# Kernel optimization log

Measured on AMD Instinct MI355X. Metric: run time of the kernel, lower is better.

Reference implementation:

```python
import jax, jax.numpy as jnp
import numpy as np

BN_EPS = 1e-5


def three_nn(unknown, known):
    # squared pairwise distances via gemm form: ||u||^2 + ||k||^2 - 2 u.k
    # unknown: (B, n, 3), known: (B, m, 3) -> d: (B, n, m)
    u2 = jnp.sum(unknown * unknown, axis=-1, keepdims=True)          # (B, n, 1)
    k2 = jnp.sum(known * known, axis=-1)[:, None, :]                 # (B, 1, m)
    d = u2 + k2 - 2.0 * jnp.einsum('bnc,bmc->bnm', unknown, known)   # (B, n, m)
    neg_d, idx = jax.lax.top_k(-d, 3)                                # 3 smallest
    return -neg_d, idx                                               # (B,n,3), (B,n,3) int32


def three_interpolate(known_feats, idx, weight):
    # known_feats: (B, C, m), idx/weight: (B, n, 3) -> (B, C, n)
    g = jnp.take_along_axis(known_feats[:, :, None, :], idx[:, None, :, :], axis=3)  # (B,C,n,3)
    return jnp.sum(g * weight[:, None, :, :], axis=3)


def conv1x1(x, W, b):
    # x: (B, C_in, N), W: (C_out, C_in), b: (C_out,)
    return jnp.einsum('oc,bcn->bon', W, x) + b[None, :, None]


def batchnorm(x, gamma, beta):
    # training-mode BN over (B, N) per channel, biased variance
    mean = jnp.mean(x, axis=(0, 2), keepdims=True)
    var = jnp.mean((x - mean) ** 2, axis=(0, 2), keepdims=True)
    xn = (x - mean) * jax.lax.rsqrt(var + BN_EPS)
    return xn * gamma[None, :, None] + beta[None, :, None]


def setup_inputs() -> dict:
    key = jax.random.key(0)
    ks = jax.random.split(key, 16)
    B, n, m = 16, 4096, 1024
    C1, C2, C = 128, 256, 256  # in_channels, known feat channels (=mlp[0]), mlp width
    inp = {
        'unknown': jax.random.normal(ks[0], (B, n, 3), jnp.float32),
        'known': jax.random.normal(ks[1], (B, m, 3), jnp.float32),
        'unknow_feats': jax.random.normal(ks[2], (B, C1, n), jnp.float32),
        'known_feats': jax.random.normal(ks[3], (B, C2, m), jnp.float32),
        # mlp_unknow: Conv1d(C1->C) + BN (no relu)
        'Wu': jax.random.normal(ks[4], (C, C1), jnp.float32) * (1.0 / np.sqrt(C1)),
        'bu': jnp.zeros((C,), jnp.float32),
        'gu': jnp.ones((C,), jnp.float32),
        'betau': jnp.zeros((C,), jnp.float32),
        # mlp_convs[0]: Conv1d(C->C) + BN + relu
        'W1': jax.random.normal(ks[5], (C, C), jnp.float32) * (1.0 / np.sqrt(C)),
        'b1': jnp.zeros((C,), jnp.float32),
        'g1': jnp.ones((C,), jnp.float32),
        'beta1': jnp.zeros((C,), jnp.float32),
        # mlp_convs[1]: Conv1d(C->C) + BN + relu
        'W2': jax.random.normal(ks[6], (C, C), jnp.float32) * (1.0 / np.sqrt(C)),
        'b2': jnp.zeros((C,), jnp.float32),
        'g2': jnp.ones((C,), jnp.float32),
        'beta2': jnp.zeros((C,), jnp.float32),
    }
    return inp


def reference(unknown, known, unknow_feats, known_feats,
              Wu, bu, gu, betau, W1, b1, g1, beta1, W2, b2, g2, beta2):
    dist, idx = three_nn(unknown, known)            # squared dists (B,n,3)
    dist_recip = 1.0 / (dist + 1e-8)
    norm = jnp.sum(dist_recip, axis=2, keepdims=True)
    weight = dist_recip / norm
    interpolated = three_interpolate(known_feats, idx, weight)   # (B, 256, n)

    skip = batchnorm(conv1x1(unknow_feats, Wu, bu), gu, betau)   # (B, 256, n)
    x = interpolated + skip
    x = jax.nn.relu(batchnorm(conv1x1(x, W1, b1), g1, beta1))
    x = jax.nn.relu(batchnorm(conv1x1(x, W2, b2), g2, beta2))
    return x
```

## Files before the change

### kernel.cpp

```cpp
#include <hip/hip_runtime.h>
#include <hip/hip_bf16.h>
#include <cstddef>
#include <cstdint>

#define BATCH 16
#define NPTS  4096
#define MPTS  1024
#define PTOT  65536
#define C1    128
#define C2    256

typedef short bf16x8 __attribute__((ext_vector_type(8)));
typedef float f32x4  __attribute__((ext_vector_type(4)));
typedef unsigned int u32x4 __attribute__((ext_vector_type(4)));

static __device__ __forceinline__ float bf2f(unsigned int u16) {
    union { unsigned int i; float f; } v; v.i = u16 << 16; return v.f;
}
static __device__ __forceinline__ unsigned short f2bf(float f) {
    union { float f; unsigned int i; } v; v.f = f;
    unsigned int u = v.i;
    return (unsigned short)((u + 0x7FFFu + ((u >> 16) & 1u)) >> 16);
}

static __device__ __forceinline__ void st_wt_b128(void* p, u32x4 v) {
    asm volatile("global_store_dwordx4 %0, %1, off sc0 sc1" :: "v"(p), "v"(v) : "memory");
}
static __device__ __forceinline__ void st_wt_f128(void* p, f32x4 v) {
    asm volatile("global_store_dwordx4 %0, %1, off sc0 sc1" :: "v"(p), "v"(v) : "memory");
}
static __device__ __forceinline__ void st_wt_b64(void* p, uint2 v) {
    asm volatile("global_store_dwordx2 %0, %1, off sc0 sc1" :: "v"(p), "v"(v) : "memory");
}
static __device__ __forceinline__ void st_wt_b32(void* p, unsigned v) {
    asm volatile("global_store_dword %0, %1, off sc0 sc1" :: "v"(p), "v"(v) : "memory");
}
static __device__ __forceinline__ void st_wt_b16(void* p, unsigned v) {
    asm volatile("global_store_short %0, %1, off sc0 sc1" :: "v"(p), "v"(v) : "memory");
}

template <int SWZ>
__global__ void k_transpose(const float* __restrict__ in, unsigned short* __restrict__ out,
                            int C, int N) {
    __shared__ float tile[64][65];
    int b  = blockIdx.z;
    int n0 = blockIdx.x * 64;
    int c0 = blockIdx.y * 64;
    const float* src = in + (size_t)b * C * N;
    unsigned short* dst = out + (size_t)b * N * C;
    int t  = threadIdx.x;
    int t4 = t >> 6;
    int tn = t & 63;
#pragma unroll
    for (int i = 0; i < 16; ++i) {
        int cc = i * 4 + t4;
        tile[cc][tn] = src[(size_t)(c0 + cc) * N + n0 + tn];
    }
    __syncthreads();
#pragma unroll
    for (int i = 0; i < 16; ++i) {
        int nn = i * 4 + t4;
        int p  = n0 + nn;
        int c  = c0 + tn;
        size_t off;
        if (SWZ) off = (size_t)p * C + (size_t)((((c >> 3) ^ (p & 7)) << 3) + (c & 7));
        else     off = (size_t)p * C + c;
        st_wt_b16(dst + off, (unsigned)f2bf(tile[tn][nn]));
    }
}

__global__ void k_cvt_pack(const float* __restrict__ in, unsigned short* __restrict__ out, int K) {
    int tid = blockIdx.x * 256 + threadIdx.x;
    if (tid >= 256 * K) return;
    int ch = tid / K, k = tid % K;
    int ks = k >> 5, lhi = (k >> 3) & 3, e = k & 7;
    int wv = ch >> 6, i = (ch >> 4) & 3, llo = ch & 15;
    int lane = lhi * 16 + llo;
    st_wt_b16(out + ((size_t)((ks * 16 + wv * 4 + i) * 64 + lane)) * 8 + e,
              (unsigned)f2bf(in[tid]));
}

static __device__ __forceinline__ bool nn_less(float da, int ia, float db, int ib) {
    return (da < db) || (da == db && ia < ib);
}

__global__ void k_three_nn(const float* __restrict__ unknown, const float* __restrict__ known,
                           int* __restrict__ idx_out, float* __restrict__ w_out) {
    __shared__ float4 kpt[MPTS + 4];
    int t  = threadIdx.x;
    int p0 = blockIdx.x * 64;
    int b  = p0 >> 12;
    const float* kb = known + (size_t)b * MPTS * 3;
    for (int i = t; i < MPTS; i += 256) {
        float x = kb[i * 3 + 0], y = kb[i * 3 + 1], z = kb[i * 3 + 2];
        float dd = __fadd_rn(__fadd_rn(__fmul_rn(x, x), __fmul_rn(y, y)), __fmul_rn(z, z));
        float4 v; v.x = x; v.y = y; v.z = z; v.w = dd;
        kpt[i + (i >> 8)] = v;
    }
    __syncthreads();

    int q = t & 3;
    int p = p0 + (t >> 2);
    const float* up = unknown + (size_t)p * 3;
    float ux = up[0], uy = up[1], uz = up[2];
    float u2 = __fadd_rn(__fadd_rn(__fmul_rn(ux, ux), __fmul_rn(uy, uy)), __fmul_rn(uz, uz));

    float d0 = INFINITY, d1 = INFINITY, d2 = INFINITY;
    int   i0 = 0, i1 = 0, i2 = 0;
    int base = q * 257;
#pragma unroll 4
    for (int it = 0; it < 256; ++it) {
        float4 kp = kpt[base + it];
        float dot = __fadd_rn(__fadd_rn(__fmul_rn(ux, kp.x), __fmul_rn(uy, kp.y)),
                              __fmul_rn(uz, kp.z));
        float d = __fsub_rn(__fadd_rn(u2, kp.w), __fmul_rn(2.0f, dot));
        int k = q * 256 + it;
        if (d < d0)      { d2 = d1; i2 = i1; d1 = d0; i1 = i0; d0 = d; i0 = k; }
        else if (d < d1) { d2 = d1; i2 = i1; d1 = d;  i1 = k; }
        else if (d < d2) { d2 = d;  i2 = k; }
    }

#pragma unroll
    for (int m = 1; m <= 2; m <<= 1) {
        float e0 = __shfl_xor(d0, m, 64), e1 = __shfl_xor(d1, m, 64), e2 = __shfl_xor(d2, m, 64);
        int   j0 = __shfl_xor(i0, m, 64), j1 = __shfl_xor(i1, m, 64), j2 = __shfl_xor(i2, m, 64);
        float a0 = d0, a1 = d1, a2 = d2; int x0 = i0, x1 = i1, x2 = i2;
        float b0 = e0, b1 = e1, b2 = e2; int y0 = j0, y1 = j1, y2 = j2;
        bool tk = nn_less(a0, x0, b0, y0);
        d0 = tk ? a0 : b0; i0 = tk ? x0 : y0;
        float na0 = tk ? a1 : a0; int nx0 = tk ? x1 : x0;
        float na1 = tk ? a2 : a1; int nx1 = tk ? x2 : x1;
        float nb0 = tk ? b0 : b1; int ny0 = tk ? y0 : y1;
        float nb1 = tk ? b1 : b2; int ny1 = tk ? y1 : y2;
        tk = nn_less(na0, nx0, nb0, ny0);
        d1 = tk ? na0 : nb0; i1 = tk ? nx0 : ny0;
        float ma0 = tk ? na1 : na0; int mx0 = tk ? nx1 : nx0;
        float mb0 = tk ? nb0 : nb1; int my0 = tk ? ny0 : ny1;
        tk = nn_less(ma0, mx0, mb0, my0);
        d2 = tk ? ma0 : mb0; i2 = tk ? mx0 : my0;
    }

    if (q == 0) {
        float r0 = 1.0f / (d0 + 1e-8f), r1 = 1.0f / (d1 + 1e-8f), r2 = 1.0f / (d2 + 1e-8f);
        float norm = r0 + r1 + r2;
        size_t pg = (size_t)p;
        st_wt_b32(idx_out + pg * 3 + 0, (unsigned)i0);
        st_wt_b32(idx_out + pg * 3 + 1, (unsigned)i1);
        st_wt_b32(idx_out + pg * 3 + 2, (unsigned)i2);
        union { float f; unsigned u; } w0v, w1v, w2v;
        w0v.f = r0 / norm; w1v.f = r1 / norm; w2v.f = r2 / norm;
        st_wt_b32(w_out + pg * 3 + 0, w0v.u);
        st_wt_b32(w_out + pg * 3 + 1, w1v.u);
        st_wt_b32(w_out + pg * 3 + 2, w2v.u);
    }
}

template <int K, int APPLY>
__global__ void k_gemm(
        const unsigned short* __restrict__ Wp,
        const unsigned short* __restrict__ X,
        const float* __restrict__ bias,
        const float* __restrict__ aff_a,
        const float* __restrict__ aff_c,
        unsigned short* __restrict__ Y,
        float* __restrict__ partial) {
    constexpr int NK = K / 32;
    constexpr int TILE_BYTES = 64 * K * 2;
    constexpr int SMEM_BYTES = TILE_BYTES > 32768 ? TILE_BYTES : 32768;
    __shared__ char smem[SMEM_BYTES];

    const int t    = threadIdx.x;
    const int p0   = blockIdx.x * 64;
    const int wv   = t >> 6;
    const int lane = t & 63;
    const int lhi  = lane >> 4, llo = lane & 15;

    if (!APPLY) {
        const char* src = (const char*)(X + (size_t)p0 * K);
        constexpr int ITERS = TILE_BYTES / (256 * 16);
#pragma unroll
        for (int i = 0; i < ITERS; ++i) {
            int off = (i * 256 + t) * 16;
            __builtin_amdgcn_global_load_lds(
                (const __attribute__((address_space(1))) unsigned int*)(src + off),
                (__attribute__((address_space(3))) unsigned int*)(smem + off),
                16, 0, 0);
        }
    } else {
        constexpr int CPR = K / 8;
#pragma unroll
        for (int i = 0; i < (64 * CPR) / 256; ++i) {
            int f   = i * 256 + t;
            int row = f / CPR, qp = f % CPR;
            int col = qp ^ (row & 7);
            uint4 v = *(const uint4*)(X + (size_t)(p0 + row) * K + qp * 8);
            unsigned int w[4] = {v.x, v.y, v.z, v.w};
            float4 a0 = *(const float4*)(aff_a + col * 8);
            float4 a1 = *(const float4*)(aff_a + col * 8 + 4);
            float4 cc0 = *(const float4*)(aff_c + col * 8);
            float4 cc1 = *(const float4*)(aff_c + col * 8 + 4);
            float aa[8] = {a0.x, a0.y, a0.z, a0.w, a1.x, a1.y, a1.z, a1.w};
            float cc[8] = {cc0.x, cc0.y, cc0.z, cc0.w, cc1.x, cc1.y, cc1.z, cc1.w};
#pragma unroll
            for (int q2 = 0; q2 < 4; ++q2) {
                float lo = fmaxf(bf2f(w[q2] & 0xffff) * aa[q2 * 2]     + cc[q2 * 2],     0.0f);
                float hi = fmaxf(bf2f(w[q2] >> 16)    * aa[q2 * 2 + 1] + cc[q2 * 2 + 1], 0.0f);
                w[q2] = (unsigned int)f2bf(lo) | ((unsigned int)f2bf(hi) << 16);
            }
            uint4 o; o.x = w[0]; o.y = w[1]; o.z = w[2]; o.w = w[3];
            *(uint4*)(smem + row * (K * 2) + qp * 16) = o;
        }
    }

    const unsigned short* wbase = Wp + ((size_t)(wv * 256) + lane) * 8;
    bf16x8 wA[4], wB[4];
#pragma unroll
    for (int i = 0; i < 4; ++i)
        wA[i] = *(const bf16x8*)(wbase + i * 512);

    __syncthreads();

    f32x4 acc[4][4];
#pragma unroll
    for (int i = 0; i < 4; ++i)
#pragma unroll
        for (int j = 0; j < 4; ++j) acc[i][j] = (f32x4){0.f, 0.f, 0.f, 0.f};

#pragma unroll
    for (int ks = 0; ks < NK; ks += 2) {
#pragma unroll
        for (int i = 0; i < 4; ++i)
            wB[i] = *(const bf16x8*)(wbase + (size_t)(ks + 1) * 8192 + i * 512);
        {
            bf16x8 bb[4];
#pragma unroll
            for (int j = 0; j < 4; ++j) {
                int row = j * 16 + llo;
                int cp  = (ks * 4 + lhi) ^ (row & 7);
                bb[j] = *(const bf16x8*)(smem + row * (K * 2) + cp * 16);
            }
#pragma unroll
            for (int i = 0; i < 4; ++i)
#pragma unroll
                for (int j = 0; j < 4; ++j)
                    acc[i][j] = __builtin_amdgcn_mfma_f32_16x16x32_bf16(wA[i], bb[j], acc[i][j], 0, 0, 0);
        }
        if (ks + 2 < NK) {
#pragma unroll
            for (int i = 0; i < 4; ++i)
                wA[i] = *(const bf16x8*)(wbase + (size_t)(ks + 2) * 8192 + i * 512);
        }
        {
            bf16x8 bb[4];
#pragma unroll
            for (int j = 0; j < 4; ++j) {
                int row = j * 16 + llo;
                int cp  = ((ks + 1) * 4 + lhi) ^ (row & 7);
                bb[j] = *(const bf16x8*)(smem + row * (K * 2) + cp * 16);
            }
#pragma unroll
            for (int i = 0; i < 4; ++i)
#pragma unroll
                for (int j = 0; j < 4; ++j)
                    acc[i][j] = __builtin_amdgcn_mfma_f32_16x16x32_bf16(wB[i], bb[j], acc[i][j], 0, 0, 0);
        }
    }

    __syncthreads();
#pragma unroll
    for (int i = 0; i < 4; ++i) {
        int cbase = wv * 64 + i * 16 + lhi * 4;
        float4 bv = *(const float4*)(bias + cbase);
        int c8 = cbase >> 3, hf = lhi & 1;
        float s0 = 0.f, s1 = 0.f, s2 = 0.f, s3 = 0.f;
        float q0 = 0.f, q1 = 0.f, q2 = 0.f, q3 = 0.f;
#pragma unroll
        for (int j = 0; j < 4; ++j) {
            int row = j * 16 + llo;
            float y0 = acc[i][j][0] + bv.x;
            float y1 = acc[i][j][1] + bv.y;
            float y2 = acc[i][j][2] + bv.z;
            float y3 = acc[i][j][3] + bv.w;
            s0 += y0; q0 += y0 * y0;  s1 += y1; q1 += y1 * y1;
            s2 += y2; q2 += y2 * y2;  s3 += y3; q3 += y3 * y3;
            unsigned int lo = (unsigned int)f2bf(y0) | ((unsigned int)f2bf(y1) << 16);
            unsigned int hi = (unsigned int)f2bf(y2) | ((unsigned int)f2bf(y3) << 16);
            uint2 o; o.x = lo; o.y = hi;
            *(uint2*)(smem + row * 512 + ((c8 ^ (row & 7)) << 4) + hf * 8) = o;
        }
#pragma unroll
        for (int m = 1; m <= 8; m <<= 1) {
            s0 += __shfl_xor(s0, m, 64); q0 += __shfl_xor(q0, m, 64);
            s1 += __shfl_xor(s1, m, 64); q1 += __shfl_xor(q1, m, 64);
            s2 += __shfl_xor(s2, m, 64); q2 += __shfl_xor(q2, m, 64);
            s3 += __shfl_xor(s3, m, 64); q3 += __shfl_xor(q3, m, 64);
        }
        if (llo == 0) {
            f32x4 sv = {s0, s1, s2, s3};
            f32x4 qv = {q0, q1, q2, q3};
            st_wt_f128(partial + (size_t)blockIdx.x * 512 + cbase, sv);
            st_wt_f128(partial + (size_t)blockIdx.x * 512 + 256 + cbase, qv);
        }
    }
    __syncthreads();
    {
        const char* ysrc = smem + wv * 8192 + lane * 16;
        char* ydst = (char*)(Y + (size_t)p0 * 256) + wv * 8192 + lane * 16;
#pragma unroll
        for (int i2 = 0; i2 < 8; ++i2) {
            u32x4 v = *(const u32x4*)(ysrc + i2 * 1024);
            st_wt_b128(ydst + i2 * 1024, v);
        }
    }
}

__global__ void k_red1(const float* __restrict__ partial, float* __restrict__ partA) {
    int t = threadIdx.x, g = blockIdx.x;
    float s = 0.f, q = 0.f;
#pragma unroll
    for (int i = 0; i < 16; ++i) {
        const float* pp = partial + (size_t)(g * 16 + i) * 512;
        s += pp[t]; q += pp[256 + t];
    }
    union { float f; unsigned u; } sv, qv; sv.f = s; qv.f = q;
    st_wt_b32(partA + g * 512 + t, sv.u);
    st_wt_b32(partA + g * 512 + 256 + t, qv.u);
}

__global__ void k_finalize(const float* __restrict__ partA, const float* __restrict__ gamma,
                           const float* __restrict__ beta, float* __restrict__ aff_a,
                           float* __restrict__ aff_c) {
    int c = threadIdx.x;
    float s = 0.f, q = 0.f;
#pragma unroll 8
    for (int i = 0; i < 64; ++i) { s += partA[i * 512 + c]; q += partA[i * 512 + 256 + c]; }
    float mean = s * (1.0f / PTOT);
    float var  = fmaxf(q * (1.0f / PTOT) - mean * mean, 0.0f);
    float a    = gamma[c] / sqrtf(var + 1e-5f);
    union { float f; unsigned u; } av, cv;
    av.f = a; cv.f = beta[c] - mean * a;
    st_wt_b32(aff_a + c, av.u);
    st_wt_b32(aff_c + c, cv.u);
}

__global__ void k_build_x(const unsigned short* __restrict__ y0, const unsigned short* __restrict__ kfT,
                          const int* __restrict__ idx, const float* __restrict__ wgt,
                          const float* __restrict__ aff_a, const float* __restrict__ aff_c,
                          unsigned short* __restrict__ X) {
    int t   = threadIdx.x;
    int p   = blockIdx.x * 8 + (t >> 5);
    int col = t & 31;
    int c0  = col * 8;
    int b   = p >> 12;
    int pos = col ^ (p & 7);
    int i0 = idx[p * 3 + 0], i1 = idx[p * 3 + 1], i2 = idx[p * 3 + 2];
    float w0 = wgt[p * 3 + 0], w1 = wgt[p * 3 + 1], w2 = wgt[p * 3 + 2];
    const size_t kb = (size_t)b * MPTS * C2;
    uint4 v0 = *(const uint4*)(kfT + kb + (size_t)i0 * C2 + c0);
    uint4 v1 = *(const uint4*)(kfT + kb + (size_t)i1 * C2 + c0);
    uint4 v2 = *(const uint4*)(kfT + kb + (size_t)i2 * C2 + c0);
    uint4 vy = *(const uint4*)(y0 + (size_t)p * C2 + pos * 8);
    const unsigned int* u0 = (const unsigned int*)&v0;
    const unsigned int* u1 = (const unsigned int*)&v1;
    const unsigned int* u2 = (const unsigned int*)&v2;
    const unsigned int* uy = (const unsigned int*)&vy;
    unsigned int r[4];
#pragma unroll
    for (int q = 0; q < 4; ++q) {
        int c = c0 + q * 2;
        float lo = w0 * bf2f(u0[q] & 0xffff) + w1 * bf2f(u1[q] & 0xffff) + w2 * bf2f(u2[q] & 0xffff)
                 + bf2f(uy[q] & 0xffff) * aff_a[c] + aff_c[c];
        float hi = w0 * bf2f(u0[q] >> 16) + w1 * bf2f(u1[q] >> 16) + w2 * bf2f(u2[q] >> 16)
                 + bf2f(uy[q] >> 16) * aff_a[c + 1] + aff_c[c + 1];
        r[q] = (unsigned int)f2bf(lo) | ((unsigned int)f2bf(hi) << 16);
    }
    u32x4 vout; vout.x = r[0]; vout.y = r[1]; vout.z = r[2]; vout.w = r[3];
    st_wt_b128(X + (size_t)p * C2 + pos * 8, vout);
}

__global__ void k_final(const unsigned short* __restrict__ Y2, const float* __restrict__ aff_a,
                        const float* __restrict__ aff_c, float* __restrict__ out) {
    __shared__ float tile[64][65];
    int p0 = blockIdx.x * 64;
    int c0 = blockIdx.y * 64;
    int t  = threadIdx.x;
    int t4 = t >> 6, t64 = t & 63;
#pragma unroll
    for (int i = 0; i < 16; ++i) {
        int r = i * 4 + t4;
        int p = p0 + r;
        int c = c0 + t64;
        float v = bf2f(Y2[(size_t)p * 256 + (((c >> 3) ^ (p & 7)) << 3) + (c & 7)])
                  * aff_a[c] + aff_c[c];
        tile[t64][r] = fmaxf(v, 0.0f);
    }
    __syncthreads();
    int b   = p0 >> 12;
    int pin = p0 & 4095;
#pragma unroll
    for (int i = 0; i < 16; ++i) {
        int cc = i * 4 + t4;
        __builtin_nontemporal_store(tile[cc][t64],
            out + ((size_t)b * 256 + c0 + cc) * 4096 + pin + t64);
    }
}

extern "C" void kernel_launch(void* const* d_in, const int* in_sizes, int n_in,
                              void* d_out, int out_size, void* d_ws, size_t ws_size,
                              hipStream_t stream) {
    const float* unknown = (const float*)d_in[0];
    const float* known   = (const float*)d_in[1];
    const float* ufeat   = (const float*)d_in[2];
    const float* kfeat   = (const float*)d_in[3];
    const float* Wu      = (const float*)d_in[4];
    const float* bu      = (const float*)d_in[5];
    const float* gu      = (const float*)d_in[6];
    const float* betau   = (const float*)d_in[7];
    const float* W1      = (const float*)d_in[8];
    const float* b1      = (const float*)d_in[9];
    const float* g1      = (const float*)d_in[10];
    const float* beta1   = (const float*)d_in[11];
    const float* W2      = (const float*)d_in[12];
    const float* b2      = (const float*)d_in[13];
    const float* g2      = (const float*)d_in[14];
    const float* beta2   = (const float*)d_in[15];
    float* out = (float*)d_out;

    char* ws = (char*)d_ws;
    unsigned short* reg0 = (unsigned short*)ws;
    unsigned short* ybuf = (unsigned short*)(ws + ((size_t)32 << 20));
    unsigned short* kfT  = (unsigned short*)(ws + ((size_t)64 << 20));
    unsigned short* Wub  = (unsigned short*)(ws + ((size_t)72 << 20));
    unsigned short* W1b  = Wub + 256 * 128;
    unsigned short* W2b  = W1b + 256 * 256;
    int*   idxb = (int*)(W2b + 256 * 256);
    float* wgtb = (float*)(idxb + (size_t)PTOT * 3);
    float* affa0 = wgtb + (size_t)PTOT * 3;
    float* affc0 = affa0 + 256;
    float* affa1 = affc0 + 256;
    float* affc1 = affa1 + 256;
    float* affa2 = affc1 + 256;
    float* affc2 = affa2 + 256;
    float* part0  = (float*)(ws + ((size_t)16 << 20));
    float* partA0 = (float*)(ws + ((size_t)18 << 20));
    float* part12  = (float*)(ws + ((size_t)64 << 20));
    float* partA12 = (float*)(ws + ((size_t)66 << 20));
    if (ws_size < ((size_t)75 << 20)) return;

    k_transpose<1><<<dim3(NPTS / 64, C1 / 64, BATCH), 256, 0, stream>>>(ufeat, reg0, C1, NPTS);
    k_transpose<0><<<dim3(MPTS / 64, C2 / 64, BATCH), 256, 0, stream>>>(kfeat, kfT, C2, MPTS);
    k_cvt_pack<<<128, 256, 0, stream>>>(Wu, Wub, 128);
    k_cvt_pack<<<256, 256, 0, stream>>>(W1, W1b, 256);
    k_cvt_pack<<<256, 256, 0, stream>>>(W2, W2b, 256);

    k_three_nn<<<PTOT / 64, 256, 0, stream>>>(unknown, known, idxb, wgtb);

    k_gemm<C1, 0><<<PTOT / 64, 256, 0, stream>>>(Wub, reg0, bu, nullptr, nullptr, ybuf, part0);
    k_red1<<<64, 256, 0, stream>>>(part0, partA0);
    k_finalize<<<1, 256, 0, stream>>>(partA0, gu, betau, affa0, affc0);

    k_build_x<<<PTOT / 8, 256, 0, stream>>>(ybuf, kfT, idxb, wgtb, affa0, affc0, reg0);

    k_gemm<C2, 0><<<PTOT / 64, 256, 0, stream>>>(W1b, reg0, b1, nullptr, nullptr, ybuf, part12);
    k_red1<<<64, 256, 0, stream>>>(part12, partA12);
    k_finalize<<<1, 256, 0, stream>>>(partA12, g1, beta1, affa1, affc1);

    k_gemm<C2, 1><<<PTOT / 64, 256, 0, stream>>>(W2b, ybuf, b2, affa1, affc1, reg0, part12);
    k_red1<<<64, 256, 0, stream>>>(part12, partA12);
    k_finalize<<<1, 256, 0, stream>>>(partA12, g2, beta2, affa2, affc2);

    k_final<<<dim3(PTOT / 64, 4), 256, 0, stream>>>(reg0, affa2, affc2, out);

    (void)in_sizes; (void)n_in; (void)out_size;
}
```

Baseline: 209.0 us.

## Shrink GEMM point tile to 16 and fuse input transpose into first conv GEMM

The conv GEMM now processes 16 points per block instead of 64, with a single B fragment per k-step, 8 KB of shared memory and launch bounds aimed at higher occupancy. A new mode reads the fp32 channel-major unknown features directly, converts them to bf16 and swizzles them into shared memory, which removes the separate transpose kernel and its round trip through global memory. The partial-statistics reduction is adjusted for four times as many blocks, and one write-through store becomes a plain store. The trade-off is that each weight fragment loaded from global memory now feeds only 16 points, so weight traffic per point rises and MFMA reuse falls.

```diff
diff --git a/kernel.cpp b/kernel.cpp
--- a/kernel.cpp
+++ b/kernel.cpp
@@ -28,9 +28,6 @@
 }
 static __device__ __forceinline__ void st_wt_f128(void* p, f32x4 v) {
     asm volatile("global_store_dwordx4 %0, %1, off sc0 sc1" :: "v"(p), "v"(v) : "memory");
-}
-static __device__ __forceinline__ void st_wt_b64(void* p, uint2 v) {
-    asm volatile("global_store_dwordx2 %0, %1, off sc0 sc1" :: "v"(p), "v"(v) : "memory");
 }
 static __device__ __forceinline__ void st_wt_b32(void* p, unsigned v) {
     asm volatile("global_store_dword %0, %1, off sc0 sc1" :: "v"(p), "v"(v) : "memory");
@@ -155,29 +152,29 @@
     }
 }
 
-template <int K, int APPLY>
-__global__ void k_gemm(
+template <int K, int MODE>
+__global__ __launch_bounds__(256, 4) void k_gemm(
         const unsigned short* __restrict__ Wp,
         const unsigned short* __restrict__ X,
+        const float* __restrict__ Xf,
         const float* __restrict__ bias,
         const float* __restrict__ aff_a,
         const float* __restrict__ aff_c,
         unsigned short* __restrict__ Y,
         float* __restrict__ partial) {
     constexpr int NK = K / 32;
-    constexpr int TILE_BYTES = 64 * K * 2;
-    constexpr int SMEM_BYTES = TILE_BYTES > 32768 ? TILE_BYTES : 32768;
-    __shared__ char smem[SMEM_BYTES];
+    constexpr int TB = 16 * K * 2;
+    __shared__ char smem[8192];
 
     const int t    = threadIdx.x;
-    const int p0   = blockIdx.x * 64;
+    const int p0   = blockIdx.x * 16;
     const int wv   = t >> 6;
     const int lane = t & 63;
     const int lhi  = lane >> 4, llo = lane & 15;
 
-    if (!APPLY) {
+    if (MODE == 0) {
         const char* src = (const char*)(X + (size_t)p0 * K);
-        constexpr int ITERS = TILE_BYTES / (256 * 16);
+        constexpr int ITERS = TB / (256 * 16);
 #pragma unroll
         for (int i = 0; i < ITERS; ++i) {
             int off = (i * 256 + t) * 16;
@@ -186,10 +183,10 @@
                 (__attribute__((address_space(3))) unsigned int*)(smem + off),
                 16, 0, 0);
         }
-    } else {
+    } else if (MODE == 1) {
         constexpr int CPR = K / 8;
 #pragma unroll
-        for (int i = 0; i < (64 * CPR) / 256; ++i) {
+        for (int i = 0; i < (16 * CPR) / 256; ++i) {
             int f   = i * 256 + t;
             int row = f / CPR, qp = f % CPR;
             int col = qp ^ (row & 7);
@@ -210,6 +207,20 @@
             uint4 o; o.x = w[0]; o.y = w[1]; o.z = w[2]; o.w = w[3];
             *(uint4*)(smem + row * (K * 2) + qp * 16) = o;
         }
+    } else {
+        int c    = t >> 1;
+        int half = (t & 1) * 8;
+        int b    = p0 >> 12;
+        const float* src = Xf + ((size_t)b * C1 + c) * NPTS + (p0 & 4095) + half;
+        float4 v0 = *(const float4*)(src);
+        float4 v1 = *(const float4*)(src + 4);
+        float fv[8] = {v0.x, v0.y, v0.z, v0.w, v1.x, v1.y, v1.z, v1.w};
+#pragma unroll
+        for (int e = 0; e < 8; ++e) {
+            int p = half + e;
+            *(unsigned short*)(smem + p * (K * 2) +
+                               ((((c >> 3) ^ (p & 7)) << 4) + (c & 7) * 2)) = f2bf(fv[e]);
+        }
     }
 
     const unsigned short* wbase = Wp + ((size_t)(wv * 256) + lane) * 8;
@@ -220,11 +231,9 @@
 
     __syncthreads();
 
-    f32x4 acc[4][4];
-#pragma unroll
-    for (int i = 0; i < 4; ++i)
-#pragma unroll
-        for (int j = 0; j < 4; ++j) acc[i][j] = (f32x4){0.f, 0.f, 0.f, 0.f};
+    f32x4 acc[4];
+#pragma unroll
+    for (int i = 0; i < 4; ++i) acc[i] = (f32x4){0.f, 0.f, 0.f, 0.f};
 
 #pragma unroll
     for (int ks = 0; ks < NK; ks += 2) {
@@ -232,18 +241,11 @@
         for (int i = 0; i < 4; ++i)
             wB[i] = *(const bf16x8*)(wbase + (size_t)(ks + 1) * 8192 + i * 512);
         {
-            bf16x8 bb[4];
-#pragma unroll
-            for (int j = 0; j < 4; ++j) {
-                int row = j * 16 + llo;
-                int cp  = (ks * 4 + lhi) ^ (row & 7);
-                bb[j] = *(const bf16x8*)(smem + row * (K * 2) + cp * 16);
-            }
+            int cp = (ks * 4 + lhi) ^ (llo & 7);
+            bf16x8 bb = *(const bf16x8*)(smem + llo * (K * 2) + cp * 16);
 #pragma unroll
             for (int i = 0; i < 4; ++i)
-#pragma unroll
-                for (int j = 0; j < 4; ++j)
-                    acc[i][j] = __builtin_amdgcn_mfma_f32_16x16x32_bf16(wA[i], bb[j], acc[i][j], 0, 0, 0);
+                acc[i] = __builtin_amdgcn_mfma_f32_16x16x32_bf16(wA[i], bb, acc[i], 0, 0, 0);
         }
         if (ks + 2 < NK) {
 #pragma unroll
@@ -251,18 +253,11 @@
                 wA[i] = *(const bf16x8*)(wbase + (size_t)(ks + 2) * 8192 + i * 512);
         }
         {
-            bf16x8 bb[4];
-#pragma unroll
-            for (int j = 0; j < 4; ++j) {
-                int row = j * 16 + llo;
-                int cp  = ((ks + 1) * 4 + lhi) ^ (row & 7);
-                bb[j] = *(const bf16x8*)(smem + row * (K * 2) + cp * 16);
-            }
+            int cp = ((ks + 1) * 4 + lhi) ^ (llo & 7);
+            bf16x8 bb = *(const bf16x8*)(smem + llo * (K * 2) + cp * 16);
 #pragma unroll
             for (int i = 0; i < 4; ++i)
-#pragma unroll
-                for (int j = 0; j < 4; ++j)
-                    acc[i][j] = __builtin_amdgcn_mfma_f32_16x16x32_bf16(wB[i], bb[j], acc[i][j], 0, 0, 0);
+                acc[i] = __builtin_amdgcn_mfma_f32_16x16x32_bf16(wB[i], bb, acc[i], 0, 0, 0);
         }
     }
 
@@ -272,22 +267,19 @@
         int cbase = wv * 64 + i * 16 + lhi * 4;
         float4 bv = *(const float4*)(bias + cbase);
         int c8 = cbase >> 3, hf = lhi & 1;
-        float s0 = 0.f, s1 = 0.f, s2 = 0.f, s3 = 0.f;
-        float q0 = 0.f, q1 = 0.f, q2 = 0.f, q3 = 0.f;
-#pragma unroll
-        for (int j = 0; j < 4; ++j) {
-            int row = j * 16 + llo;
-            float y0 = acc[i][j][0] + bv.x;
-            float y1 = acc[i][j][1] + bv.y;
-            float y2 = acc[i][j][2] + bv.z;
-            float y3 = acc[i][j][3] + bv.w;
-            s0 += y0; q0 += y0 * y0;  s1 += y1; q1 += y1 * y1;
-            s2 += y2; q2 += y2 * y2;  s3 += y3; q3 += y3 * y3;
-            unsigned int lo = (unsigned int)f2bf(y0) | ((unsigned int)f2bf(y1) << 16);
-            unsigned int hi = (unsigned int)f2bf(y2) | ((unsigned int)f2bf(y3) << 16);
-            uint2 o; o.x = lo; o.y = hi;
-            *(uint2*)(smem + row * 512 + ((c8 ^ (row & 7)) << 4) + hf * 8) = o;
-        }
+        int row = llo;
+        float y0 = acc[i][0] + bv.x;
+        float y1 = acc[i][1] + bv.y;
+        float y2 = acc[i][2] + bv.z;
+        float y3 = acc[i][3] + bv.w;
+        float s0 = y0, q0 = y0 * y0;
+        float s1 = y1, q1 = y1 * y1;
+        float s2 = y2, q2 = y2 * y2;
+        float s3 = y3, q3 = y3 * y3;
+        unsigned int lo = (unsigned int)f2bf(y0) | ((unsigned int)f2bf(y1) << 16);
+        unsigned int hi = (unsigned int)f2bf(y2) | ((unsigned int)f2bf(y3) << 16);
+        uint2 o; o.x = lo; o.y = hi;
+        *(uint2*)(smem + row * 512 + ((c8 ^ (row & 7)) << 4) + hf * 8) = o;
 #pragma unroll
         for (int m = 1; m <= 8; m <<= 1) {
             s0 += __shfl_xor(s0, m, 64); q0 += __shfl_xor(q0, m, 64);
@@ -304,22 +296,21 @@
     }
     __syncthreads();
     {
-        const char* ysrc = smem + wv * 8192 + lane * 16;
-        char* ydst = (char*)(Y + (size_t)p0 * 256) + wv * 8192 + lane * 16;
-#pragma unroll
-        for (int i2 = 0; i2 < 8; ++i2) {
-            u32x4 v = *(const u32x4*)(ysrc + i2 * 1024);
-            st_wt_b128(ydst + i2 * 1024, v);
-        }
+        const char* ysrc = smem + t * 32;
+        char* ydst = (char*)(Y + (size_t)p0 * 256) + t * 32;
+        u32x4 v0 = *(const u32x4*)(ysrc);
+        u32x4 v1 = *(const u32x4*)(ysrc + 16);
+        st_wt_b128(ydst, v0);
+        st_wt_b128(ydst + 16, v1);
     }
 }
 
 __global__ void k_red1(const float* __restrict__ partial, float* __restrict__ partA) {
     int t = threadIdx.x, g = blockIdx.x;
     float s = 0.f, q = 0.f;
-#pragma unroll
-    for (int i = 0; i < 16; ++i) {
-        const float* pp = partial + (size_t)(g * 16 + i) * 512;
+#pragma unroll 8
+    for (int i = 0; i < 64; ++i) {
+        const float* pp = partial + (size_t)(g * 64 + i) * 512;
         s += pp[t]; q += pp[256 + t];
     }
     union { float f; unsigned u; } sv, qv; sv.f = s; qv.f = q;
@@ -374,8 +365,8 @@
                  + bf2f(uy[q] >> 16) * aff_a[c + 1] + aff_c[c + 1];
         r[q] = (unsigned int)f2bf(lo) | ((unsigned int)f2bf(hi) << 16);
     }
-    u32x4 vout; vout.x = r[0]; vout.y = r[1]; vout.z = r[2]; vout.w = r[3];
-    st_wt_b128(X + (size_t)p * C2 + pos * 8, vout);
+    uint4 vout; vout.x = r[0]; vout.y = r[1]; vout.z = r[2]; vout.w = r[3];
+    *(uint4*)(X + (size_t)p * C2 + pos * 8) = vout;
 }
 
 __global__ void k_final(const unsigned short* __restrict__ Y2, const float* __restrict__ aff_a,
@@ -441,13 +432,11 @@
     float* affc1 = affa1 + 256;
     float* affa2 = affc1 + 256;
     float* affc2 = affa2 + 256;
+    float* partA = affc2 + 256;
     float* part0  = (float*)(ws + ((size_t)16 << 20));
-    float* partA0 = (float*)(ws + ((size_t)18 << 20));
-    float* part12  = (float*)(ws + ((size_t)64 << 20));
-    float* partA12 = (float*)(ws + ((size_t)66 << 20));
+    float* part12 = (float*)(ws + ((size_t)64 << 20));
     if (ws_size < ((size_t)75 << 20)) return;
 
-    k_transpose<1><<<dim3(NPTS / 64, C1 / 64, BATCH), 256, 0, stream>>>(ufeat, reg0, C1, NPTS);
     k_transpose<0><<<dim3(MPTS / 64, C2 / 64, BATCH), 256, 0, stream>>>(kfeat, kfT, C2, MPTS);
     k_cvt_pack<<<128, 256, 0, stream>>>(Wu, Wub, 128);
     k_cvt_pack<<<256, 256, 0, stream>>>(W1, W1b, 256);
@@ -455,19 +444,22 @@
 
     k_three_nn<<<PTOT / 64, 256, 0, stream>>>(unknown, known, idxb, wgtb);
 
-    k_gemm<C1, 0><<<PTOT / 64, 256, 0, stream>>>(Wub, reg0, bu, nullptr, nullptr, ybuf, part0);
-    k_red1<<<64, 256, 0, stream>>>(part0, partA0);
-    k_finalize<<<1, 256, 0, stream>>>(partA0, gu, betau, affa0, affc0);
+    k_gemm<C1, 2><<<PTOT / 16, 256, 0, stream>>>(Wub, nullptr, ufeat, bu, nullptr, nullptr,
+                                                 ybuf, part0);
+    k_red1<<<64, 256, 0, stream>>>(part0, partA);
+    k_finalize<<<1, 256, 0, stream>>>(partA, gu, betau, affa0, affc0);
 
     k_build_x<<<PTOT / 8, 256, 0, stream>>>(ybuf, kfT, idxb, wgtb, affa0, affc0, reg0);
 
-    k_gemm<C2, 0><<<PTOT / 64, 256, 0, stream>>>(W1b, reg0, b1, nullptr, nullptr, ybuf, part12);
-    k_red1<<<64, 256, 0, stream>>>(part12, partA12);
-    k_finalize<<<1, 256, 0, stream>>>(partA12, g1, beta1, affa1, affc1);
-
-    k_gemm<C2, 1><<<PTOT / 64, 256, 0, stream>>>(W2b, ybuf, b2, affa1, affc1, reg0, part12);
-    k_red1<<<64, 256, 0, stream>>>(part12, partA12);
-    k_finalize<<<1, 256, 0, stream>>>(partA12, g2, beta2, affa2, affc2);
+    k_gemm<C2, 0><<<PTOT / 16, 256, 0, stream>>>(W1b, reg0, nullptr, b1, nullptr, nullptr,
+                                                 ybuf, part12);
+    k_red1<<<64, 256, 0, stream>>>(part12, partA);
+    k_finalize<<<1, 256, 0, stream>>>(partA, g1, beta1, affa1, affc1);
+
+    k_gemm<C2, 1><<<PTOT / 16, 256, 0, stream>>>(W2b, ybuf, nullptr, b2, affa1, affc1,
+                                                 reg0, part12);
+    k_red1<<<64, 256, 0, stream>>>(part12, partA);
+    k_finalize<<<1, 256, 0, stream>>>(partA, g2, beta2, affa2, affc2);
 
     k_final<<<dim3(PTOT / 64, 4), 256, 0, stream>>>(reg0, affa2, affc2, out);
 
```

Result: slower. 228.8 us (+9.5%).

## Fuse input transpose and interpolation gather into GEMM prologues, halve point tile

Applied to the files above, without the earlier changes.

Removes the separate unknown-feature transpose and build_x kernels. The first GEMM now reads fp32 features directly, converting to bf16 into swizzled shared memory. The second GEMM gathers the three-NN features and applies the skip BN affine in its prologue. The point tile per block drops from 64 to 32 with launch bounds for 4 blocks per CU, which doubles the number of blocks and partial-sum rows that k_red1 must reduce. Partial sums are placed in the output buffer and workspace reuse is reshuffled, cutting intermediate global traffic at the cost of more redundant weight loads per point.

```diff
diff --git a/kernel.cpp b/kernel.cpp
--- a/kernel.cpp
+++ b/kernel.cpp
@@ -28,9 +28,6 @@
 }
 static __device__ __forceinline__ void st_wt_f128(void* p, f32x4 v) {
     asm volatile("global_store_dwordx4 %0, %1, off sc0 sc1" :: "v"(p), "v"(v) : "memory");
-}
-static __device__ __forceinline__ void st_wt_b64(void* p, uint2 v) {
-    asm volatile("global_store_dwordx2 %0, %1, off sc0 sc1" :: "v"(p), "v"(v) : "memory");
 }
 static __device__ __forceinline__ void st_wt_b32(void* p, unsigned v) {
     asm volatile("global_store_dword %0, %1, off sc0 sc1" :: "v"(p), "v"(v) : "memory");
@@ -155,41 +152,32 @@
     }
 }
 
-template <int K, int APPLY>
-__global__ void k_gemm(
+template <int K, int MODE>
+__global__ __launch_bounds__(256, 4) void k_gemm(
         const unsigned short* __restrict__ Wp,
         const unsigned short* __restrict__ X,
+        const float* __restrict__ Xf,
+        const unsigned short* __restrict__ kfT,
+        const int* __restrict__ idx,
+        const float* __restrict__ wgt,
         const float* __restrict__ bias,
         const float* __restrict__ aff_a,
         const float* __restrict__ aff_c,
         unsigned short* __restrict__ Y,
         float* __restrict__ partial) {
     constexpr int NK = K / 32;
-    constexpr int TILE_BYTES = 64 * K * 2;
-    constexpr int SMEM_BYTES = TILE_BYTES > 32768 ? TILE_BYTES : 32768;
-    __shared__ char smem[SMEM_BYTES];
+    __shared__ char smem[34816];
 
     const int t    = threadIdx.x;
-    const int p0   = blockIdx.x * 64;
+    const int p0   = blockIdx.x * 32;
     const int wv   = t >> 6;
     const int lane = t & 63;
     const int lhi  = lane >> 4, llo = lane & 15;
 
-    if (!APPLY) {
-        const char* src = (const char*)(X + (size_t)p0 * K);
-        constexpr int ITERS = TILE_BYTES / (256 * 16);
-#pragma unroll
-        for (int i = 0; i < ITERS; ++i) {
-            int off = (i * 256 + t) * 16;
-            __builtin_amdgcn_global_load_lds(
-                (const __attribute__((address_space(1))) unsigned int*)(src + off),
-                (__attribute__((address_space(3))) unsigned int*)(smem + off),
-                16, 0, 0);
-        }
-    } else {
+    if (MODE == 1) {
         constexpr int CPR = K / 8;
 #pragma unroll
-        for (int i = 0; i < (64 * CPR) / 256; ++i) {
+        for (int i = 0; i < (32 * CPR) / 256; ++i) {
             int f   = i * 256 + t;
             int row = f / CPR, qp = f % CPR;
             int col = qp ^ (row & 7);
@@ -210,6 +198,59 @@
             uint4 o; o.x = w[0]; o.y = w[1]; o.z = w[2]; o.w = w[3];
             *(uint4*)(smem + row * (K * 2) + qp * 16) = o;
         }
+    } else if (MODE == 2) {
+        int c    = t >> 1;
+        int half = (t & 1) * 16;
+        int b    = p0 >> 12;
+        const float* src = Xf + ((size_t)b * C1 + c) * NPTS + (p0 & 4095) + half;
+#pragma unroll
+        for (int k4 = 0; k4 < 4; ++k4) {
+            float4 v = *(const float4*)(src + k4 * 4);
+            float fv[4] = {v.x, v.y, v.z, v.w};
+#pragma unroll
+            for (int e = 0; e < 4; ++e) {
+                int p = half + k4 * 4 + e;
+                *(unsigned short*)(smem + p * (K * 2) +
+                                   ((((c >> 3) ^ (p & 7)) << 4) + (c & 7) * 2)) = f2bf(fv[e]);
+            }
+        }
+    } else {
+        int pj  = t >> 3;
+        int sub = t & 7;
+        int p   = p0 + pj;
+        int b   = p >> 12;
+        int i0 = idx[p * 3 + 0], i1 = idx[p * 3 + 1], i2 = idx[p * 3 + 2];
+        float w0 = wgt[p * 3 + 0], w1 = wgt[p * 3 + 1], w2 = wgt[p * 3 + 2];
+        const unsigned short* kb = kfT + (size_t)b * MPTS * C2;
+#pragma unroll
+        for (int cc2 = 0; cc2 < 4; ++cc2) {
+            int cc = sub * 4 + cc2;
+            int cbase = cc * 8;
+            u32x4 v0 = *(const u32x4*)(kb + (size_t)i0 * C2 + cbase);
+            u32x4 v1 = *(const u32x4*)(kb + (size_t)i1 * C2 + cbase);
+            u32x4 v2 = *(const u32x4*)(kb + (size_t)i2 * C2 + cbase);
+            int pos = cc ^ (p & 7);
+            u32x4 vy = *(const u32x4*)(X + (size_t)p * C2 + pos * 8);
+            float4 a0 = *(const float4*)(aff_a + cbase);
+            float4 a1 = *(const float4*)(aff_a + cbase + 4);
+            float4 c0f = *(const float4*)(aff_c + cbase);
+            float4 c1f = *(const float4*)(aff_c + cbase + 4);
+            float aa[8] = {a0.x, a0.y, a0.z, a0.w, a1.x, a1.y, a1.z, a1.w};
+            float cf[8] = {c0f.x, c0f.y, c0f.z, c0f.w, c1f.x, c1f.y, c1f.z, c1f.w};
+            unsigned r[4];
+#pragma unroll
+            for (int qq = 0; qq < 4; ++qq) {
+                float lo = w0 * bf2f(v0[qq] & 0xffff) + w1 * bf2f(v1[qq] & 0xffff)
+                         + w2 * bf2f(v2[qq] & 0xffff)
+                         + bf2f(vy[qq] & 0xffff) * aa[qq * 2] + cf[qq * 2];
+                float hi = w0 * bf2f(v0[qq] >> 16) + w1 * bf2f(v1[qq] >> 16)
+                         + w2 * bf2f(v2[qq] >> 16)
+                         + bf2f(vy[qq] >> 16) * aa[qq * 2 + 1] + cf[qq * 2 + 1];
+                r[qq] = (unsigned)f2bf(lo) | ((unsigned)f2bf(hi) << 16);
+            }
+            u32x4 vo; vo.x = r[0]; vo.y = r[1]; vo.z = r[2]; vo.w = r[3];
+            *(u32x4*)(smem + pj * 512 + pos * 16) = vo;
+        }
     }
 
     const unsigned short* wbase = Wp + ((size_t)(wv * 256) + lane) * 8;
@@ -220,11 +261,11 @@
 
     __syncthreads();
 
-    f32x4 acc[4][4];
+    f32x4 acc[4][2];
 #pragma unroll
     for (int i = 0; i < 4; ++i)
 #pragma unroll
-        for (int j = 0; j < 4; ++j) acc[i][j] = (f32x4){0.f, 0.f, 0.f, 0.f};
+        for (int j = 0; j < 2; ++j) acc[i][j] = (f32x4){0.f, 0.f, 0.f, 0.f};
 
 #pragma unroll
     for (int ks = 0; ks < NK; ks += 2) {
@@ -232,9 +273,9 @@
         for (int i = 0; i < 4; ++i)
             wB[i] = *(const bf16x8*)(wbase + (size_t)(ks + 1) * 8192 + i * 512);
         {
-            bf16x8 bb[4];
-#pragma unroll
-            for (int j = 0; j < 4; ++j) {
+            bf16x8 bb[2];
+#pragma unroll
+            for (int j = 0; j < 2; ++j) {
                 int row = j * 16 + llo;
                 int cp  = (ks * 4 + lhi) ^ (row & 7);
                 bb[j] = *(const bf16x8*)(smem + row * (K * 2) + cp * 16);
@@ -242,7 +283,7 @@
 #pragma unroll
             for (int i = 0; i < 4; ++i)
 #pragma unroll
-                for (int j = 0; j < 4; ++j)
+                for (int j = 0; j < 2; ++j)
                     acc[i][j] = __builtin_amdgcn_mfma_f32_16x16x32_bf16(wA[i], bb[j], acc[i][j], 0, 0, 0);
         }
         if (ks + 2 < NK) {
@@ -251,9 +292,9 @@
                 wA[i] = *(const bf16x8*)(wbase + (size_t)(ks + 2) * 8192 + i * 512);
         }
         {
-            bf16x8 bb[4];
-#pragma unroll
-            for (int j = 0; j < 4; ++j) {
+            bf16x8 bb[2];
+#pragma unroll
+            for (int j = 0; j < 2; ++j) {
                 int row = j * 16 + llo;
                 int cp  = ((ks + 1) * 4 + lhi) ^ (row & 7);
                 bb[j] = *(const bf16x8*)(smem + row * (K * 2) + cp * 16);
@@ -261,7 +302,7 @@
 #pragma unroll
             for (int i = 0; i < 4; ++i)
 #pragma unroll
-                for (int j = 0; j < 4; ++j)
+                for (int j = 0; j < 2; ++j)
                     acc[i][j] = __builtin_amdgcn_mfma_f32_16x16x32_bf16(wB[i], bb[j], acc[i][j], 0, 0, 0);
         }
     }
@@ -275,7 +316,7 @@
         float s0 = 0.f, s1 = 0.f, s2 = 0.f, s3 = 0.f;
         float q0 = 0.f, q1 = 0.f, q2 = 0.f, q3 = 0.f;
 #pragma unroll
-        for (int j = 0; j < 4; ++j) {
+        for (int j = 0; j < 2; ++j) {
             int row = j * 16 + llo;
             float y0 = acc[i][j][0] + bv.x;
             float y1 = acc[i][j][1] + bv.y;
@@ -304,12 +345,12 @@
     }
     __syncthreads();
     {
-        const char* ysrc = smem + wv * 8192 + lane * 16;
-        char* ydst = (char*)(Y + (size_t)p0 * 256) + wv * 8192 + lane * 16;
-#pragma unroll
-        for (int i2 = 0; i2 < 8; ++i2) {
-            u32x4 v = *(const u32x4*)(ysrc + i2 * 1024);
-            st_wt_b128(ydst + i2 * 1024, v);
+        const char* ysrc = smem + t * 16;
+        char* ydst = (char*)(Y + (size_t)p0 * 256) + t * 16;
+#pragma unroll
+        for (int i2 = 0; i2 < 4; ++i2) {
+            u32x4 v = *(const u32x4*)(ysrc + i2 * 4096);
+            st_wt_b128(ydst + i2 * 4096, v);
         }
     }
 }
@@ -317,9 +358,9 @@
 __global__ void k_red1(const float* __restrict__ partial, float* __restrict__ partA) {
     int t = threadIdx.x, g = blockIdx.x;
     float s = 0.f, q = 0.f;
-#pragma unroll
-    for (int i = 0; i < 16; ++i) {
-        const float* pp = partial + (size_t)(g * 16 + i) * 512;
+#pragma unroll 8
+    for (int i = 0; i < 32; ++i) {
+        const float* pp = partial + (size_t)(g * 32 + i) * 512;
         s += pp[t]; q += pp[256 + t];
     }
     union { float f; unsigned u; } sv, qv; sv.f = s; qv.f = q;
@@ -341,41 +382,6 @@
     av.f = a; cv.f = beta[c] - mean * a;
     st_wt_b32(aff_a + c, av.u);
     st_wt_b32(aff_c + c, cv.u);
-}
-
-__global__ void k_build_x(const unsigned short* __restrict__ y0, const unsigned short* __restrict__ kfT,
-                          const int* __restrict__ idx, const float* __restrict__ wgt,
-                          const float* __restrict__ aff_a, const float* __restrict__ aff_c,
-                          unsigned short* __restrict__ X) {
-    int t   = threadIdx.x;
-    int p   = blockIdx.x * 8 + (t >> 5);
-    int col = t & 31;
-    int c0  = col * 8;
-    int b   = p >> 12;
-    int pos = col ^ (p & 7);
-    int i0 = idx[p * 3 + 0], i1 = idx[p * 3 + 1], i2 = idx[p * 3 + 2];
-    float w0 = wgt[p * 3 + 0], w1 = wgt[p * 3 + 1], w2 = wgt[p * 3 + 2];
-    const size_t kb = (size_t)b * MPTS * C2;
-    uint4 v0 = *(const uint4*)(kfT + kb + (size_t)i0 * C2 + c0);
-    uint4 v1 = *(const uint4*)(kfT + kb + (size_t)i1 * C2 + c0);
-    uint4 v2 = *(const uint4*)(kfT + kb + (size_t)i2 * C2 + c0);
-    uint4 vy = *(const uint4*)(y0 + (size_t)p * C2 + pos * 8);
-    const unsigned int* u0 = (const unsigned int*)&v0;
-    const unsigned int* u1 = (const unsigned int*)&v1;
-    const unsigned int* u2 = (const unsigned int*)&v2;
-    const unsigned int* uy = (const unsigned int*)&vy;
-    unsigned int r[4];
-#pragma unroll
-    for (int q = 0; q < 4; ++q) {
-        int c = c0 + q * 2;
-        float lo = w0 * bf2f(u0[q] & 0xffff) + w1 * bf2f(u1[q] & 0xffff) + w2 * bf2f(u2[q] & 0xffff)
-                 + bf2f(uy[q] & 0xffff) * aff_a[c] + aff_c[c];
-        float hi = w0 * bf2f(u0[q] >> 16) + w1 * bf2f(u1[q] >> 16) + w2 * bf2f(u2[q] >> 16)
-                 + bf2f(uy[q] >> 16) * aff_a[c + 1] + aff_c[c + 1];
-        r[q] = (unsigned int)f2bf(lo) | ((unsigned int)f2bf(hi) << 16);
-    }
-    u32x4 vout; vout.x = r[0]; vout.y = r[1]; vout.z = r[2]; vout.w = r[3];
-    st_wt_b128(X + (size_t)p * C2 + pos * 8, vout);
 }
 
 __global__ void k_final(const unsigned short* __restrict__ Y2, const float* __restrict__ aff_a,
@@ -441,13 +447,11 @@
     float* affc1 = affa1 + 256;
     float* affa2 = affc1 + 256;
     float* affc2 = affa2 + 256;
-    float* part0  = (float*)(ws + ((size_t)16 << 20));
-    float* partA0 = (float*)(ws + ((size_t)18 << 20));
-    float* part12  = (float*)(ws + ((size_t)64 << 20));
-    float* partA12 = (float*)(ws + ((size_t)66 << 20));
+    float* partA = affc2 + 256;
+    float* part0  = (float*)ws;
+    float* partD  = (float*)d_out;
     if (ws_size < ((size_t)75 << 20)) return;
 
-    k_transpose<1><<<dim3(NPTS / 64, C1 / 64, BATCH), 256, 0, stream>>>(ufeat, reg0, C1, NPTS);
     k_transpose<0><<<dim3(MPTS / 64, C2 / 64, BATCH), 256, 0, stream>>>(kfeat, kfT, C2, MPTS);
     k_cvt_pack<<<128, 256, 0, stream>>>(Wu, Wub, 128);
     k_cvt_pack<<<256, 256, 0, stream>>>(W1, W1b, 256);
@@ -455,21 +459,22 @@
 
     k_three_nn<<<PTOT / 64, 256, 0, stream>>>(unknown, known, idxb, wgtb);
 
-    k_gemm<C1, 0><<<PTOT / 64, 256, 0, stream>>>(Wub, reg0, bu, nullptr, nullptr, ybuf, part0);
-    k_red1<<<64, 256, 0, stream>>>(part0, partA0);
-    k_finalize<<<1, 256, 0, stream>>>(partA0, gu, betau, affa0, affc0);
-
-    k_build_x<<<PTOT / 8, 256, 0, stream>>>(ybuf, kfT, idxb, wgtb, affa0, affc0, reg0);
-
-    k_gemm<C2, 0><<<PTOT / 64, 256, 0, stream>>>(W1b, reg0, b1, nullptr, nullptr, ybuf, part12);
-    k_red1<<<64, 256, 0, stream>>>(part12, partA12);
-    k_finalize<<<1, 256, 0, stream>>>(partA12, g1, beta1, affa1, affc1);
-
-    k_gemm<C2, 1><<<PTOT / 64, 256, 0, stream>>>(W2b, ybuf, b2, affa1, affc1, reg0, part12);
-    k_red1<<<64, 256, 0, stream>>>(part12, partA12);
-    k_finalize<<<1, 256, 0, stream>>>(partA12, g2, beta2, affa2, affc2);
-
-    k_final<<<dim3(PTOT / 64, 4), 256, 0, stream>>>(reg0, affa2, affc2, out);
+    k_gemm<C1, 2><<<PTOT / 32, 256, 0, stream>>>(Wub, nullptr, ufeat, nullptr, nullptr, nullptr,
+                                                 bu, nullptr, nullptr, ybuf, part0);
+    k_red1<<<64, 256, 0, stream>>>(part0, partA);
+    k_finalize<<<1, 256, 0, stream>>>(partA, gu, betau, affa0, affc0);
+
+    k_gemm<C2, 3><<<PTOT / 32, 256, 0, stream>>>(W1b, ybuf, nullptr, kfT, idxb, wgtb,
+                                                 b1, affa0, affc0, reg0, partD);
+    k_red1<<<64, 256, 0, stream>>>(partD, partA);
+    k_finalize<<<1, 256, 0, stream>>>(partA, g1, beta1, affa1, affc1);
+
+    k_gemm<C2, 1><<<PTOT / 32, 256, 0, stream>>>(W2b, reg0, nullptr, nullptr, nullptr, nullptr,
+                                                 b2, affa1, affc1, ybuf, partD);
+    k_red1<<<64, 256, 0, stream>>>(partD, partA);
+    k_finalize<<<1, 256, 0, stream>>>(partA, g2, beta2, affa2, affc2);
+
+    k_final<<<dim3(PTOT / 64, 4), 256, 0, stream>>>(ybuf, affa2, affc2, out);
 
     (void)in_sizes; (void)n_in; (void)out_size;
 }
```

Result: faster. 203.3 us (-2.7%).
